# Kernel optimization log

Hardware: AMD Instinct MI355X
Metric: run time of the kernel (lower is better)

Reference implementation:

```python
import jax, jax.numpy as jnp
import numpy as np

B, N, D = 4, 4096, 1024
QK = D // 8          # qk_dim_div = 8 -> 128
E = 2 * D            # expand_factor = 2 -> 2048


def setup_inputs() -> dict:
    key = jax.random.key(0)
    k1, k2, k3 = jax.random.split(key, 3)
    x = jax.random.normal(k1, (B, N, D), dtype=jnp.float32)
    # xavier-uniform-like scale for the fused expand / project weights
    expand = jax.random.normal(k2, (D, 2 * QK + 2 * E), dtype=jnp.float32) * np.sqrt(2.0 / (D + 2 * QK + 2 * E)).astype(np.float32)
    project = jax.random.normal(k3, (E, D), dtype=jnp.float32) * np.sqrt(2.0 / (E + D)).astype(np.float32)
    position_bias_mult = jnp.float32(4.0)
    return {"x": x, "expand": expand, "project": project, "position_bias_mult": position_bias_mult}


def _layer_norm(x, eps=1e-5):
    mu = jnp.mean(x, axis=-1, keepdims=True)
    var = jnp.mean(jnp.square(x - mu), axis=-1, keepdims=True)
    return (x - mu) * jax.lax.rsqrt(var + eps)


def reference(x, expand, project, position_bias_mult):
    d = x.shape[-1]
    qk, e = d // 8, 2 * d
    n = x.shape[1]

    nx = _layer_norm(x)
    h = nx @ expand                                    # [B, N, 2*qk + 2*e]
    q = h[..., :qk]
    k = h[..., qk:2 * qk]
    linear = h[..., 2 * qk:2 * qk + e]
    pre_gelu = h[..., 2 * qk + e:]

    gated = linear * jax.nn.gelu(pre_gelu, approximate=False)  # torch F.gelu = exact erf
    local = gated[..., :e - d]                          # [B, N, e-d]
    v = gated[..., e - d:]                              # [B, N, d]

    # learned sigmoid position bias under causal mask
    pos = jnp.arange(n)
    base = (pos[None, :] - pos[:, None]).astype(x.dtype)  # j - i
    causal = pos[None, :] <= pos[:, None]
    mask = jnp.where(causal, jax.nn.sigmoid(base + position_bias_mult), -jnp.inf)

    logits = jnp.einsum('bnq,bmq->bnm', q, k) / np.sqrt(qk).astype(np.float32) + mask
    scores = jax.nn.softmax(logits, axis=-1)            # [B, N, N]
    attn = jnp.einsum('bnm,bmd->bnd', scores, v)         # [B, N, d]

    return x + jnp.concatenate([local, attn], axis=-1) @ project
```

## Files before the change

kernel.cpp:

```cpp
#include <hip/hip_runtime.h>
#include <type_traits>

typedef __bf16 bf16x8 __attribute__((ext_vector_type(8)));
typedef __bf16 bf16x4v __attribute__((ext_vector_type(4)));
typedef float f32x4 __attribute__((ext_vector_type(4)));
typedef unsigned short u16x8 __attribute__((ext_vector_type(8)));
typedef unsigned short u16x4 __attribute__((ext_vector_type(4)));

#define NSEQ 4096
#define DM 1024
#define NBATCH 4

__device__ __forceinline__ unsigned short f2bf(float f) {
  unsigned u = __float_as_uint(f);
  u += 0x7FFFu + ((u >> 16) & 1u);
  return (unsigned short)(u >> 16);
}
__device__ __forceinline__ float bf2f(unsigned short h) {
  return __uint_as_float(((unsigned)h) << 16);
}
__device__ __forceinline__ float gelu_exact(float x) {
  return 0.5f * x * (1.0f + erff(x * 0.7071067811865475f));
}

__device__ __forceinline__ void gload_lds16(const unsigned short* src,
                                            unsigned short* dst) {
  __builtin_amdgcn_global_load_lds(
      (const __attribute__((address_space(1))) unsigned int*)src,
      (__attribute__((address_space(3))) unsigned int*)dst, 16, 0, 0);
}

#define BAR() asm volatile("s_barrier" ::: "memory")
#define VMCNT8() asm volatile("s_waitcnt vmcnt(8)" ::: "memory")

__global__ __launch_bounds__(256) void ln_kernel(const float* __restrict__ x,
                                                 unsigned short* __restrict__ nx) {
  const int row = blockIdx.x;
  const int tid = threadIdx.x;
  const float4 v = reinterpret_cast<const float4*>(x + (size_t)row * DM)[tid];
  float s = v.x + v.y + v.z + v.w;
  float q = v.x * v.x + v.y * v.y + v.z * v.z + v.w * v.w;
#pragma unroll
  for (int off = 32; off > 0; off >>= 1) {
    s += __shfl_down(s, off);
    q += __shfl_down(q, off);
  }
  __shared__ float ss[4], sq[4];
  if ((tid & 63) == 0) {
    ss[tid >> 6] = s;
    sq[tid >> 6] = q;
  }
  __syncthreads();
  const float ts = ss[0] + ss[1] + ss[2] + ss[3];
  const float tq = sq[0] + sq[1] + sq[2] + sq[3];
  const float mu = ts * (1.0f / DM);
  const float var = tq * (1.0f / DM) - mu * mu;
  const float rs = rsqrtf(var + 1e-5f);
  u16x4 o;
  o[0] = f2bf((v.x - mu) * rs);
  o[1] = f2bf((v.y - mu) * rs);
  o[2] = f2bf((v.z - mu) * rs);
  o[3] = f2bf((v.w - mu) * rs);
  *reinterpret_cast<u16x4*>(nx + (size_t)row * DM + tid * 4) = o;
}

__global__ __launch_bounds__(256) void tconv_kernel(const float* __restrict__ in,
                                                    unsigned short* __restrict__ out,
                                                    int K, int N) {
  __shared__ unsigned short tile[64][72];
  const int n0 = blockIdx.x * 64;
  const int k0 = blockIdx.y * 64;
  const int tid = threadIdx.x;
  const int lr = tid >> 4, lc = (tid & 15) * 4;
#pragma unroll
  for (int p = 0; p < 4; p++) {
    const int r = lr + p * 16;
    float4 v = *reinterpret_cast<const float4*>(in + (size_t)(k0 + r) * N + n0 + lc);
    tile[r][lc + 0] = f2bf(v.x);
    tile[r][lc + 1] = f2bf(v.y);
    tile[r][lc + 2] = f2bf(v.z);
    tile[r][lc + 3] = f2bf(v.w);
  }
  __syncthreads();
  const int nn = tid >> 2, kkg = (tid & 3) * 16;
  u16x8 o0, o1;
#pragma unroll
  for (int j = 0; j < 8; j++) {
    o0[j] = tile[kkg + j][nn];
    o1[j] = tile[kkg + 8 + j][nn];
  }
  unsigned short* dst = out + (size_t)(n0 + nn) * K + k0 + kkg;
  *reinterpret_cast<u16x8*>(dst) = o0;
  *reinterpret_cast<u16x8*>(dst + 8) = o1;
}

template <bool FINAL>
__global__ __launch_bounds__(512, 2) void gemm256_kernel(
    const unsigned short* __restrict__ A, int lda,
    const unsigned short* __restrict__ Bt, int ldb, void* __restrict__ Cv,
    int ldc, int K, int ntn, const float* __restrict__ X) {
  __shared__ unsigned short Ah[2][2][8192];
  __shared__ unsigned short Bh[2][2][8192];
  const int tid = threadIdx.x;
  const int lane = tid & 63;
  const int w = tid >> 6;
  const int lq = lane & 15;
  const int lg = lane >> 4;
  const int wm = w >> 2;
  const int wn = w & 3;
  const int bid = blockIdx.x;
  const int m0 = (bid / ntn) * 256;
  const int n0 = (bid % ntn) * 256;
  const int nk = K >> 6;

  const int g0 = w * 64 + lane;
  const int rowS = g0 >> 2;
  const int kcS = ((g0 & 3) * 8) ^ (((rowS >> 1) & 3) << 3);
  const unsigned short* Asrc = A + (size_t)(m0 + rowS) * lda + kcS;
  const unsigned short* Bsrc = Bt + (size_t)(n0 + rowS) * ldb + kcS;
  const size_t ldaj = (size_t)128 * lda;
  const size_t ldbj = (size_t)128 * ldb;
  const int dstW = w * 64 * 8;

  auto stageA = [&](int db, int kh, int kt2) {
    if (kt2 < nk) {
      const unsigned short* s = Asrc + (size_t)kt2 * 64 + kh * 32;
      unsigned short* d = &Ah[db][kh][0] + dstW;
      gload_lds16(s, d);
      gload_lds16(s + ldaj, d + 4096);
    }
  };
  auto stageB = [&](int db, int kh, int kt2) {
    if (kt2 < nk) {
      const unsigned short* s = Bsrc + (size_t)kt2 * 64 + kh * 32;
      unsigned short* d = &Bh[db][kh][0] + dstW;
      gload_lds16(s, d);
      gload_lds16(s + ldbj, d + 4096);
    }
  };

  f32x4 acc[8][4];
#pragma unroll
  for (int i = 0; i < 8; i++)
#pragma unroll
    for (int j = 0; j < 4; j++)
#pragma unroll
      for (int r = 0; r < 4; r++) acc[i][j][r] = 0.0f;

  stageA(0, 0, 0);
  stageB(0, 0, 0);
  stageA(0, 1, 0);
  stageB(0, 1, 0);
  stageA(1, 0, 1);
  stageB(1, 0, 1);
  VMCNT8();
  BAR();

  const int aBase = wm * 128;
  const int bBase = wn * 64;
  const int cSwz = (lg * 8) ^ (((lq >> 1) & 3) << 3);

#pragma unroll 1
  for (int kt = 0; kt < nk; ++kt) {
    const int buf = kt & 1;
    bf16x8 af[4], bf0[4], bf1[4];

#pragma unroll
    for (int i = 0; i < 4; i++)
      af[i] = *reinterpret_cast<const bf16x8*>(
          &Ah[buf][0][(aBase + i * 16 + lq) * 32 + cSwz]);
#pragma unroll
    for (int j = 0; j < 4; j++)
      bf0[j] = *reinterpret_cast<const bf16x8*>(
          &Bh[buf][0][(bBase + j * 16 + lq) * 32 + cSwz]);
    stageA(buf ^ 1, 1, kt + 1);
    BAR();
    __builtin_amdgcn_s_setprio(1);
#pragma unroll
    for (int i = 0; i < 4; i++)
#pragma unroll
      for (int j = 0; j < 4; j++)
        acc[i][j] =
            __builtin_amdgcn_mfma_f32_16x16x32_bf16(af[i], bf0[j], acc[i][j], 0, 0, 0);
    __builtin_amdgcn_s_setprio(0);
    BAR();

#pragma unroll
    for (int i = 0; i < 4; i++)
      af[i] = *reinterpret_cast<const bf16x8*>(
          &Ah[buf][0][(aBase + 64 + i * 16 + lq) * 32 + cSwz]);
    stageB(buf ^ 1, 1, kt + 1);
    VMCNT8();
    BAR();
    __builtin_amdgcn_s_setprio(1);
#pragma unroll
    for (int i = 0; i < 4; i++)
#pragma unroll
      for (int j = 0; j < 4; j++)
        acc[4 + i][j] = __builtin_amdgcn_mfma_f32_16x16x32_bf16(af[i], bf0[j],
                                                                acc[4 + i][j], 0, 0, 0);
    __builtin_amdgcn_s_setprio(0);
    BAR();

#pragma unroll
    for (int i = 0; i < 4; i++)
      af[i] = *reinterpret_cast<const bf16x8*>(
          &Ah[buf][1][(aBase + i * 16 + lq) * 32 + cSwz]);
#pragma unroll
    for (int j = 0; j < 4; j++)
      bf1[j] = *reinterpret_cast<const bf16x8*>(
          &Bh[buf][1][(bBase + j * 16 + lq) * 32 + cSwz]);
    stageA(buf, 0, kt + 2);
    BAR();
    __builtin_amdgcn_s_setprio(1);
#pragma unroll
    for (int i = 0; i < 4; i++)
#pragma unroll
      for (int j = 0; j < 4; j++)
        acc[i][j] =
            __builtin_amdgcn_mfma_f32_16x16x32_bf16(af[i], bf1[j], acc[i][j], 0, 0, 0);
    __builtin_amdgcn_s_setprio(0);
    BAR();

#pragma unroll
    for (int i = 0; i < 4; i++)
      af[i] = *reinterpret_cast<const bf16x8*>(
          &Ah[buf][1][(aBase + 64 + i * 16 + lq) * 32 + cSwz]);
    stageB(buf, 0, kt + 2);
    VMCNT8();
    BAR();
    __builtin_amdgcn_s_setprio(1);
#pragma unroll
    for (int i = 0; i < 4; i++)
#pragma unroll
      for (int j = 0; j < 4; j++)
        acc[4 + i][j] = __builtin_amdgcn_mfma_f32_16x16x32_bf16(af[i], bf1[j],
                                                                acc[4 + i][j], 0, 0, 0);
    __builtin_amdgcn_s_setprio(0);
    BAR();
  }

  if (FINAL) {
    float* C = reinterpret_cast<float*>(Cv);
#pragma unroll
    for (int I = 0; I < 8; I++)
#pragma unroll
      for (int j = 0; j < 4; j++)
#pragma unroll
        for (int r = 0; r < 4; r++) {
          const int row = m0 + wm * 128 + I * 16 + lg * 4 + r;
          const int col = n0 + wn * 64 + j * 16 + lq;
          const size_t off = (size_t)row * ldc + col;
          C[off] = X[off] + acc[I][j][r];
        }
  } else {
    unsigned short* C = reinterpret_cast<unsigned short*>(Cv);
#pragma unroll
    for (int I = 0; I < 8; I++)
#pragma unroll
      for (int j = 0; j < 4; j++)
#pragma unroll
        for (int r = 0; r < 4; r++) {
          const int row = m0 + wm * 128 + I * 16 + lg * 4 + r;
          const int col = n0 + wn * 64 + j * 16 + lq;
          C[(size_t)row * ldc + col] = f2bf(acc[I][j][r]);
        }
  }
}

__global__ __launch_bounds__(256) void gate_local_kernel(
    const unsigned short* __restrict__ gateH, unsigned short* __restrict__ concat) {
  const int idx = blockIdx.x * 256 + threadIdx.x;
  const int row = idx >> 7;
  const int cg = idx & 127;
  const unsigned short* hr = gateH + (size_t)row * 4096;
  u16x8 lin = *reinterpret_cast<const u16x8*>(hr + cg * 8);
  u16x8 pg = *reinterpret_cast<const u16x8*>(hr + 2048 + cg * 8);
  u16x8 o;
#pragma unroll
  for (int j = 0; j < 8; j++) {
    const float l = bf2f(lin[j]);
    const float g = gelu_exact(bf2f(pg[j]));
    o[j] = f2bf(l * g);
  }
  *reinterpret_cast<u16x8*>(concat + (size_t)row * 2048 + cg * 8) = o;
}

__global__ __launch_bounds__(256) void gate_vt_kernel(
    const unsigned short* __restrict__ gateH, unsigned short* __restrict__ vT) {
  __shared__ unsigned short tbuf[64][72];
  const int n0 = blockIdx.x * 64;
  const int d0 = blockIdx.y * 64;
  const int b = blockIdx.z;
  const int tid = threadIdx.x;
#pragma unroll
  for (int p = 0; p < 2; p++) {
    const int r = p * 32 + (tid >> 3);
    const int cg = tid & 7;
    const unsigned short* hr = gateH + (size_t)(b * NSEQ + n0 + r) * 4096;
    u16x8 lin = *reinterpret_cast<const u16x8*>(hr + 1024 + d0 + cg * 8);
    u16x8 pg = *reinterpret_cast<const u16x8*>(hr + 3072 + d0 + cg * 8);
    u16x8 o;
#pragma unroll
    for (int j = 0; j < 8; j++) {
      const float l = bf2f(lin[j]);
      const float g = gelu_exact(bf2f(pg[j]));
      o[j] = f2bf(l * g);
    }
    *reinterpret_cast<u16x8*>(&tbuf[r][cg * 8]) = o;
  }
  __syncthreads();
#pragma unroll
  for (int p = 0; p < 2; p++) {
    const int d = p * 32 + (tid >> 3);
    const int ng = tid & 7;
    u16x8 o;
#pragma unroll
    for (int j = 0; j < 8; j++) o[j] = tbuf[ng * 8 + j][d];
    *reinterpret_cast<u16x8*>(vT + (size_t)(b * DM + d0 + d) * NSEQ + n0 +
                              ng * 8) = o;
  }
}

#define P_TILE 16384
#define P_PER_B 8650752
__global__ __launch_bounds__(512, 4) void pk_kernel(
    const unsigned short* __restrict__ qk, const float* __restrict__ pbm_ptr,
    unsigned short* __restrict__ P, float* __restrict__ l) {
  __shared__ unsigned short Ks[128][136];
  const int tid = threadIdx.x;
  const int lane = tid & 63;
  const int w = tid >> 6;
  const int lq = lane & 15;
  const int lg = lane >> 4;
  const int bid = blockIdx.x;
  const int b = bid / 528;
  const int t = bid - b * 528;
  int qt = (int)((sqrtf((float)(8 * t + 1)) - 1.0f) * 0.5f);
  while ((qt + 1) * (qt + 2) / 2 <= t) ++qt;
  while (qt * (qt + 1) / 2 > t) --qt;
  const int kt = t - qt * (qt + 1) / 2;
  const float pbm = *pbm_ptr;
  const float SCALE = 0.08838834764831845f;

  const unsigned short* qb = qk + (size_t)b * NSEQ * 256;

#pragma unroll
  for (int p = 0; p < 4; p++) {
    const int task = tid + p * 512;
    const int row = task >> 4;
    const int ch = task & 15;
    bf16x8 v = *reinterpret_cast<const bf16x8*>(
        qb + (size_t)(kt * 128 + row) * 256 + 128 + ch * 8);
    *reinterpret_cast<bf16x8*>(&Ks[row][ch * 8]) = v;
  }
  const int qloc = w * 16 + lq;
  bf16x8 qf[4];
#pragma unroll
  for (int ks = 0; ks < 4; ks++)
    qf[ks] = *reinterpret_cast<const bf16x8*>(
        qb + (size_t)(qt * 128 + qloc) * 256 + ks * 32 + lg * 8);
  __syncthreads();

  f32x4 sa[8];
#pragma unroll
  for (int sub = 0; sub < 8; sub++)
#pragma unroll
    for (int r = 0; r < 4; r++) sa[sub][r] = 0.0f;
#pragma unroll
  for (int ks = 0; ks < 4; ks++)
#pragma unroll
    for (int sub = 0; sub < 8; sub++) {
      bf16x8 kf =
          *reinterpret_cast<const bf16x8*>(&Ks[sub * 16 + lq][ks * 32 + lg * 8]);
      sa[sub] = __builtin_amdgcn_mfma_f32_16x16x32_bf16(kf, qf[ks], sa[sub], 0, 0, 0);
    }
  const size_t KL = (size_t)(qt + 1) * 128;
  unsigned short* Prow = P + (size_t)b * P_PER_B +
                         (size_t)(qt * (qt + 1) / 2) * P_TILE + (size_t)qloc * KL +
                         kt * 128;
  float ps = 0.0f;
  const bool diag = (kt == qt);
#pragma unroll
  for (int sub = 0; sub < 8; sub++) {
    bf16x4v pv;
#pragma unroll
    for (int r = 0; r < 4; r++) {
      const int kvloc = sub * 16 + lg * 4 + r;
      float p;
      if (diag && kvloc > qloc) {
        p = 0.0f;
      } else {
        const float dn = (float)((kt - qt) * 128 + kvloc - qloc) + pbm;
        const float s = sa[sub][r] * SCALE + 1.0f / (1.0f + __expf(-dn));
        p = __expf(s);
      }
      ps += p;
      pv[r] = (__bf16)p;
    }
    *reinterpret_cast<bf16x4v*>(Prow + sub * 16 + lg * 4) = pv;
  }
  ps += __shfl_xor(ps, 16);
  ps += __shfl_xor(ps, 32);
  if (lane < 16) atomicAdd(&l[b * NSEQ + qt * 128 + w * 16 + lane], ps);
}

__global__ __launch_bounds__(256, 4) void pv_kernel(
    const unsigned short* __restrict__ P, const unsigned short* __restrict__ vT,
    const float* __restrict__ l, unsigned short* __restrict__ concat) {
  __shared__ unsigned short As[128][64];
  __shared__ unsigned short Bs[128][64];
  const int tid = threadIdx.x;
  const int bid = blockIdx.x;
  const int qt = 31 - (bid >> 5);
  const int rest = bid & 31;
  const int b = rest >> 3;
  const int nt = rest & 7;
  const int KL = (qt + 1) * 128;
  const unsigned short* A =
      P + (size_t)b * P_PER_B + (size_t)(qt * (qt + 1) / 2) * P_TILE;
  const unsigned short* Bt = vT + (size_t)b * DM * NSEQ;
  const int n0 = nt * 128;
  const int lane = tid & 63;
  const int w = tid >> 6;
  const int lr = lane & 15;
  const int lg = lane >> 4;
  const int wr = (w >> 1) * 64;
  const int wc = (w & 1) * 64;
  const int rSwz = (lr & 7) << 3;

  f32x4 acc[4][4];
#pragma unroll
  for (int i = 0; i < 4; i++)
#pragma unroll
    for (int j = 0; j < 4; j++)
#pragma unroll
      for (int r = 0; r < 4; r++) acc[i][j][r] = 0.0f;

  for (int k0 = 0; k0 < KL; k0 += 64) {
#pragma unroll
    for (int j = 0; j < 4; j++) {
      const int boff = w * 4096 + j * 1024 + lane * 16;
      const int row = boff >> 7;
      const int col = (((boff & 127) >> 1)) ^ ((row & 7) << 3);
      gload_lds16(A + (size_t)row * KL + k0 + col,
                  &As[0][0] + (boff - lane * 16) / 2);
    }
#pragma unroll
    for (int j = 0; j < 4; j++) {
      const int boff = w * 4096 + j * 1024 + lane * 16;
      const int row = boff >> 7;
      const int col = (((boff & 127) >> 1)) ^ ((row & 7) << 3);
      gload_lds16(Bt + (size_t)(n0 + row) * NSEQ + k0 + col,
                  &Bs[0][0] + (boff - lane * 16) / 2);
    }
    __syncthreads();
#pragma unroll
    for (int kk = 0; kk < 64; kk += 32) {
      bf16x8 af[4], bfr[4];
#pragma unroll
      for (int i = 0; i < 4; i++)
        af[i] = *reinterpret_cast<const bf16x8*>(
            &As[wr + i * 16 + lr][(kk + lg * 8) ^ rSwz]);
#pragma unroll
      for (int j = 0; j < 4; j++)
        bfr[j] = *reinterpret_cast<const bf16x8*>(
            &Bs[wc + j * 16 + lr][(kk + lg * 8) ^ rSwz]);
#pragma unroll
      for (int i = 0; i < 4; i++)
#pragma unroll
        for (int j = 0; j < 4; j++)
          acc[i][j] = __builtin_amdgcn_mfma_f32_16x16x32_bf16(af[i], bfr[j],
                                                              acc[i][j], 0, 0, 0);
    }
    __syncthreads();
  }

  const float* lb = l + b * NSEQ + qt * 128;
#pragma unroll
  for (int i = 0; i < 4; i++) {
    f32x4 lv = *reinterpret_cast<const f32x4*>(&lb[wr + i * 16 + lg * 4]);
    f32x4 inv;
#pragma unroll
    for (int r = 0; r < 4; r++) inv[r] = 1.0f / lv[r];
#pragma unroll
    for (int j = 0; j < 4; j++)
#pragma unroll
      for (int r = 0; r < 4; r++) {
        const int grow = b * NSEQ + qt * 128 + wr + i * 16 + lg * 4 + r;
        const int col = 1024 + n0 + wc + j * 16 + lr;
        concat[(size_t)grow * 2048 + col] = f2bf(acc[i][j][r] * inv[r]);
      }
  }
}

extern "C" void kernel_launch(void* const* d_in, const int* in_sizes, int n_in,
                              void* d_out, int out_size, void* d_ws,
                              size_t ws_size, hipStream_t stream) {
  (void)in_sizes;
  (void)n_in;
  (void)out_size;
  const float* x = (const float*)d_in[0];
  const float* expand = (const float*)d_in[1];
  const float* project = (const float*)d_in[2];
  const float* pbm = (const float*)d_in[3];
  float* out = (float*)d_out;

  const size_t QK_BYTES = (size_t)16384 * 256 * 2;
  const size_t GH_BYTES = (size_t)16384 * 4096 * 2;
  const size_t CAT_BYTES = (size_t)16384 * 2048 * 2;
  const size_t NX_BYTES = (size_t)16384 * DM * 2;
  const size_t P_BYTES = (size_t)NBATCH * P_PER_B * 2;
  if (ws_size < QK_BYTES + GH_BYTES + CAT_BYTES + NX_BYTES) return;

  char* ws = (char*)d_ws;
  unsigned short* qk = (unsigned short*)ws;
  unsigned short* gateH = (unsigned short*)(ws + QK_BYTES);
  unsigned short* concat = (unsigned short*)(ws + QK_BYTES + GH_BYTES);
  unsigned short* nx = (unsigned short*)(ws + QK_BYTES + GH_BYTES + CAT_BYTES);
  unsigned short* vT = nx;
  unsigned short* projectT = nx;
  unsigned short* expandT = concat;
  unsigned short* P = gateH;
  float* l = (float*)(ws + QK_BYTES + P_BYTES);

  tconv_kernel<<<dim3(68, 16), 256, 0, stream>>>(expand, expandT, 1024, 4352);
  ln_kernel<<<16384, 256, 0, stream>>>(x, nx);
  gemm256_kernel<false><<<dim3(64), 512, 0, stream>>>(
      nx, DM, expandT, DM, (void*)qk, 256, DM, 1, nullptr);
  gemm256_kernel<false><<<dim3(64 * 16), 512, 0, stream>>>(
      nx, DM, expandT + (size_t)256 * DM, DM, (void*)gateH, 4096, DM, 16, nullptr);
  gate_local_kernel<<<8192, 256, 0, stream>>>(gateH, concat);
  gate_vt_kernel<<<dim3(64, 16, 4), 256, 0, stream>>>(gateH, vT);
  hipMemsetAsync(l, 0, (size_t)NBATCH * NSEQ * 4, stream);
  pk_kernel<<<dim3(NBATCH * 528), 512, 0, stream>>>(qk, pbm, P, l);
  pv_kernel<<<dim3(1024), 256, 0, stream>>>(P, vT, l, concat);
  tconv_kernel<<<dim3(16, 32), 256, 0, stream>>>(project, projectT, 2048, DM);
  gemm256_kernel<true><<<dim3(64 * 4), 512, 0, stream>>>(
      concat, 2048, projectT, 2048, (void*)out, DM, 2048, 4, x);
}
```

Measured before the change: 478.0 us.

## Prefetch LDS fragments one phase ahead and remap blocks across XCDs

Restructures the GEMM main loop so LDS-to-register fragment loads for the next MFMA phase are issued right after the barrier and overlap the current phase's MFMAs, using two alternating register sets (Ax/Ay, Ba/Bb). The aim is to hide LDS read latency behind matrix-core work. It also remaps blockIdx so consecutive tiles land on the same XCD (8-way interleave) for better L2 reuse. Extra live fragment registers raise pressure, which could cause spills under the 512-thread, 2-blocks-per-CU launch bounds. The remap assumes the grid size is a multiple of 8.

```diff
diff --git a/kernel.cpp b/kernel.cpp
--- a/kernel.cpp
+++ b/kernel.cpp
@@ -108,7 +108,8 @@
   const int lg = lane >> 4;
   const int wm = w >> 2;
   const int wn = w & 3;
-  const int bid = blockIdx.x;
+  const int cpx = gridDim.x >> 3;
+  const int bid = (blockIdx.x & 7) * cpx + (blockIdx.x >> 3);
   const int m0 = (bid / ntn) * 256;
   const int n0 = (bid % ntn) * 256;
   const int nk = K >> 6;
@@ -139,6 +140,23 @@
     }
   };
 
+  const int aBase = wm * 128;
+  const int bBase = wn * 64;
+  const int cSwz = (lg * 8) ^ (((lq >> 1) & 3) << 3);
+
+  auto loadA = [&](bf16x8* dst, int bufI, int kh, int rbase) {
+#pragma unroll
+    for (int i = 0; i < 4; i++)
+      dst[i] = *reinterpret_cast<const bf16x8*>(
+          &Ah[bufI][kh][(rbase + i * 16 + lq) * 32 + cSwz]);
+  };
+  auto loadB = [&](bf16x8* dst, int bufI, int kh) {
+#pragma unroll
+    for (int j = 0; j < 4; j++)
+      dst[j] = *reinterpret_cast<const bf16x8*>(
+          &Bh[bufI][kh][(bBase + j * 16 + lq) * 32 + cSwz]);
+  };
+
   f32x4 acc[8][4];
 #pragma unroll
   for (int i = 0; i < 8; i++)
@@ -146,6 +164,8 @@
     for (int j = 0; j < 4; j++)
 #pragma unroll
       for (int r = 0; r < 4; r++) acc[i][j][r] = 0.0f;
+
+  bf16x8 Ax[4], Ay[4], Ba[4], Bb[4];
 
   stageA(0, 0, 0);
   stageB(0, 0, 0);
@@ -155,86 +175,65 @@
   stageB(1, 0, 1);
   VMCNT8();
   BAR();
-
-  const int aBase = wm * 128;
-  const int bBase = wn * 64;
-  const int cSwz = (lg * 8) ^ (((lq >> 1) & 3) << 3);
+  loadA(Ax, 0, 0, aBase);
+  loadB(Ba, 0, 0);
 
 #pragma unroll 1
   for (int kt = 0; kt < nk; ++kt) {
     const int buf = kt & 1;
-    bf16x8 af[4], bf0[4], bf1[4];
-
+
+    stageA(buf ^ 1, 1, kt + 1);
+    BAR();
+    loadA(Ay, buf, 0, aBase + 64);
+    __builtin_amdgcn_s_setprio(1);
 #pragma unroll
     for (int i = 0; i < 4; i++)
-      af[i] = *reinterpret_cast<const bf16x8*>(
-          &Ah[buf][0][(aBase + i * 16 + lq) * 32 + cSwz]);
-#pragma unroll
-    for (int j = 0; j < 4; j++)
-      bf0[j] = *reinterpret_cast<const bf16x8*>(
-          &Bh[buf][0][(bBase + j * 16 + lq) * 32 + cSwz]);
-    stageA(buf ^ 1, 1, kt + 1);
-    BAR();
-    __builtin_amdgcn_s_setprio(1);
-#pragma unroll
-    for (int i = 0; i < 4; i++)
 #pragma unroll
       for (int j = 0; j < 4; j++)
         acc[i][j] =
-            __builtin_amdgcn_mfma_f32_16x16x32_bf16(af[i], bf0[j], acc[i][j], 0, 0, 0);
+            __builtin_amdgcn_mfma_f32_16x16x32_bf16(Ax[i], Ba[j], acc[i][j], 0, 0, 0);
     __builtin_amdgcn_s_setprio(0);
     BAR();
 
-#pragma unroll
-    for (int i = 0; i < 4; i++)
-      af[i] = *reinterpret_cast<const bf16x8*>(
-          &Ah[buf][0][(aBase + 64 + i * 16 + lq) * 32 + cSwz]);
     stageB(buf ^ 1, 1, kt + 1);
     VMCNT8();
     BAR();
+    loadA(Ax, buf, 1, aBase);
+    loadB(Bb, buf, 1);
     __builtin_amdgcn_s_setprio(1);
 #pragma unroll
     for (int i = 0; i < 4; i++)
 #pragma unroll
       for (int j = 0; j < 4; j++)
-        acc[4 + i][j] = __builtin_amdgcn_mfma_f32_16x16x32_bf16(af[i], bf0[j],
+        acc[4 + i][j] = __builtin_amdgcn_mfma_f32_16x16x32_bf16(Ay[i], Ba[j],
                                                                 acc[4 + i][j], 0, 0, 0);
     __builtin_amdgcn_s_setprio(0);
     BAR();
 
+    stageA(buf, 0, kt + 2);
+    BAR();
+    loadA(Ay, buf, 1, aBase + 64);
+    __builtin_amdgcn_s_setprio(1);
 #pragma unroll
     for (int i = 0; i < 4; i++)
-      af[i] = *reinterpret_cast<const bf16x8*>(
-          &Ah[buf][1][(aBase + i * 16 + lq) * 32 + cSwz]);
-#pragma unroll
-    for (int j = 0; j < 4; j++)
-      bf1[j] = *reinterpret_cast<const bf16x8*>(
-          &Bh[buf][1][(bBase + j * 16 + lq) * 32 + cSwz]);
-    stageA(buf, 0, kt + 2);
-    BAR();
-    __builtin_amdgcn_s_setprio(1);
-#pragma unroll
-    for (int i = 0; i < 4; i++)
 #pragma unroll
       for (int j = 0; j < 4; j++)
         acc[i][j] =
-            __builtin_amdgcn_mfma_f32_16x16x32_bf16(af[i], bf1[j], acc[i][j], 0, 0, 0);
+            __builtin_amdgcn_mfma_f32_16x16x32_bf16(Ax[i], Bb[j], acc[i][j], 0, 0, 0);
     __builtin_amdgcn_s_setprio(0);
     BAR();
 
-#pragma unroll
-    for (int i = 0; i < 4; i++)
-      af[i] = *reinterpret_cast<const bf16x8*>(
-          &Ah[buf][1][(aBase + 64 + i * 16 + lq) * 32 + cSwz]);
     stageB(buf, 0, kt + 2);
     VMCNT8();
     BAR();
+    loadA(Ax, buf ^ 1, 0, aBase);
+    loadB(Ba, buf ^ 1, 0);
     __builtin_amdgcn_s_setprio(1);
 #pragma unroll
     for (int i = 0; i < 4; i++)
 #pragma unroll
       for (int j = 0; j < 4; j++)
-        acc[4 + i][j] = __builtin_amdgcn_mfma_f32_16x16x32_bf16(af[i], bf1[j],
+        acc[4 + i][j] = __builtin_amdgcn_mfma_f32_16x16x32_bf16(Ay[i], Bb[j],
                                                                 acc[4 + i][j], 0, 0, 0);
     __builtin_amdgcn_s_setprio(0);
     BAR();
```

New measurement: 490.6 us. +2.6%, slower.

## Fuse GELU gating into expand GEMM epilogue via interleaved weight columns

Applied to the files above, without the earlier changes.

The transposed expand weights get their linear and pre-gelu columns interleaved in 32-column groups. Each 64-wide warp tile of the gate GEMM then holds matching linear and gate values, so the epilogue computes linear*gelu directly and writes local features to concat and v to a compact buffer. This drops the 16384x4096 bf16 intermediate round trip and the separate gating kernels, leaving a pure transpose kernel for v. The cost is a heavier GEMM epilogue with erf, scattered 2-byte stores, and a reshuffled workspace layout.

```diff
diff --git a/kernel.cpp b/kernel.cpp
--- a/kernel.cpp
+++ b/kernel.cpp
@@ -32,6 +32,14 @@
 
 #define BAR() asm volatile("s_barrier" ::: "memory")
 #define VMCNT8() asm volatile("s_waitcnt vmcnt(8)" ::: "memory")
+
+__device__ __forceinline__ int perm_col(int n) {
+  if (n < 256) return n;
+  int c = n - 256;
+  if (c < 2048) return 256 + ((c >> 5) << 6) + (c & 31);
+  c -= 2048;
+  return 256 + ((c >> 5) << 6) + 32 + (c & 31);
+}
 
 __global__ __launch_bounds__(256) void ln_kernel(const float* __restrict__ x,
                                                  unsigned short* __restrict__ nx) {
@@ -64,6 +72,7 @@
   *reinterpret_cast<u16x4*>(nx + (size_t)row * DM + tid * 4) = o;
 }
 
+template <bool PERM>
 __global__ __launch_bounds__(256) void tconv_kernel(const float* __restrict__ in,
                                                     unsigned short* __restrict__ out,
                                                     int K, int N) {
@@ -89,16 +98,18 @@
     o0[j] = tile[kkg + j][nn];
     o1[j] = tile[kkg + 8 + j][nn];
   }
-  unsigned short* dst = out + (size_t)(n0 + nn) * K + k0 + kkg;
+  const int orow = PERM ? perm_col(n0 + nn) : (n0 + nn);
+  unsigned short* dst = out + (size_t)orow * K + k0 + kkg;
   *reinterpret_cast<u16x8*>(dst) = o0;
   *reinterpret_cast<u16x8*>(dst + 8) = o1;
 }
 
-template <bool FINAL>
+template <int MODE>
 __global__ __launch_bounds__(512, 2) void gemm256_kernel(
     const unsigned short* __restrict__ A, int lda,
     const unsigned short* __restrict__ Bt, int ldb, void* __restrict__ Cv,
-    int ldc, int K, int ntn, const float* __restrict__ X) {
+    void* __restrict__ Cv2, int ldc, int K, int ntn,
+    const float* __restrict__ X) {
   __shared__ unsigned short Ah[2][2][8192];
   __shared__ unsigned short Bh[2][2][8192];
   const int tid = threadIdx.x;
@@ -240,7 +251,7 @@
     BAR();
   }
 
-  if (FINAL) {
+  if (MODE == 1) {
     float* C = reinterpret_cast<float*>(Cv);
 #pragma unroll
     for (int I = 0; I < 8; I++)
@@ -253,7 +264,7 @@
           const size_t off = (size_t)row * ldc + col;
           C[off] = X[off] + acc[I][j][r];
         }
-  } else {
+  } else if (MODE == 0) {
     unsigned short* C = reinterpret_cast<unsigned short*>(Cv);
 #pragma unroll
     for (int I = 0; I < 8; I++)
@@ -265,29 +276,31 @@
           const int col = n0 + wn * 64 + j * 16 + lq;
           C[(size_t)row * ldc + col] = f2bf(acc[I][j][r]);
         }
-  }
-}
-
-__global__ __launch_bounds__(256) void gate_local_kernel(
-    const unsigned short* __restrict__ gateH, unsigned short* __restrict__ concat) {
-  const int idx = blockIdx.x * 256 + threadIdx.x;
-  const int row = idx >> 7;
-  const int cg = idx & 127;
-  const unsigned short* hr = gateH + (size_t)row * 4096;
-  u16x8 lin = *reinterpret_cast<const u16x8*>(hr + cg * 8);
-  u16x8 pg = *reinterpret_cast<const u16x8*>(hr + 2048 + cg * 8);
-  u16x8 o;
-#pragma unroll
-  for (int j = 0; j < 8; j++) {
-    const float l = bf2f(lin[j]);
-    const float g = gelu_exact(bf2f(pg[j]));
-    o[j] = f2bf(l * g);
-  }
-  *reinterpret_cast<u16x8*>(concat + (size_t)row * 2048 + cg * 8) = o;
-}
-
-__global__ __launch_bounds__(256) void gate_vt_kernel(
-    const unsigned short* __restrict__ gateH, unsigned short* __restrict__ vT) {
+  } else {
+    unsigned short* concat = reinterpret_cast<unsigned short*>(Cv);
+    unsigned short* vbuf = reinterpret_cast<unsigned short*>(Cv2);
+    const int pi = (n0 + wn * 64) >> 6;
+    const int cBase = pi * 32;
+#pragma unroll
+    for (int I = 0; I < 8; I++)
+#pragma unroll
+      for (int j = 0; j < 2; j++) {
+        const int c = cBase + j * 16 + lq;
+#pragma unroll
+        for (int r = 0; r < 4; r++) {
+          const int row = m0 + wm * 128 + I * 16 + lg * 4 + r;
+          const float g = acc[I][j][r] * gelu_exact(acc[I][j + 2][r]);
+          if (c < 1024)
+            concat[(size_t)row * 2048 + c] = f2bf(g);
+          else
+            vbuf[(size_t)row * 1024 + (c - 1024)] = f2bf(g);
+        }
+      }
+  }
+}
+
+__global__ __launch_bounds__(256) void vt_kernel(
+    const unsigned short* __restrict__ vbuf, unsigned short* __restrict__ vT) {
   __shared__ unsigned short tbuf[64][72];
   const int n0 = blockIdx.x * 64;
   const int d0 = blockIdx.y * 64;
@@ -297,17 +310,9 @@
   for (int p = 0; p < 2; p++) {
     const int r = p * 32 + (tid >> 3);
     const int cg = tid & 7;
-    const unsigned short* hr = gateH + (size_t)(b * NSEQ + n0 + r) * 4096;
-    u16x8 lin = *reinterpret_cast<const u16x8*>(hr + 1024 + d0 + cg * 8);
-    u16x8 pg = *reinterpret_cast<const u16x8*>(hr + 3072 + d0 + cg * 8);
-    u16x8 o;
-#pragma unroll
-    for (int j = 0; j < 8; j++) {
-      const float l = bf2f(lin[j]);
-      const float g = gelu_exact(bf2f(pg[j]));
-      o[j] = f2bf(l * g);
-    }
-    *reinterpret_cast<u16x8*>(&tbuf[r][cg * 8]) = o;
+    u16x8 v = *reinterpret_cast<const u16x8*>(
+        vbuf + (size_t)(b * NSEQ + n0 + r) * 1024 + d0 + cg * 8);
+    *reinterpret_cast<u16x8*>(&tbuf[r][cg * 8]) = v;
   }
   __syncthreads();
 #pragma unroll
@@ -507,35 +512,38 @@
   float* out = (float*)d_out;
 
   const size_t QK_BYTES = (size_t)16384 * 256 * 2;
+  const size_t VBUF_BYTES = (size_t)16384 * 1024 * 2;
+  const size_t P_BYTES = (size_t)NBATCH * P_PER_B * 2;
+  const size_t L_BYTES = (size_t)NBATCH * NSEQ * 4;
   const size_t GH_BYTES = (size_t)16384 * 4096 * 2;
   const size_t CAT_BYTES = (size_t)16384 * 2048 * 2;
   const size_t NX_BYTES = (size_t)16384 * DM * 2;
-  const size_t P_BYTES = (size_t)NBATCH * P_PER_B * 2;
   if (ws_size < QK_BYTES + GH_BYTES + CAT_BYTES + NX_BYTES) return;
 
   char* ws = (char*)d_ws;
   unsigned short* qk = (unsigned short*)ws;
-  unsigned short* gateH = (unsigned short*)(ws + QK_BYTES);
+  unsigned short* vbuf = (unsigned short*)(ws + QK_BYTES);
+  unsigned short* P = (unsigned short*)(ws + QK_BYTES + VBUF_BYTES);
+  float* l = (float*)(ws + QK_BYTES + VBUF_BYTES + P_BYTES);
+  unsigned short* expandT =
+      (unsigned short*)(ws + QK_BYTES + VBUF_BYTES + P_BYTES + L_BYTES);
   unsigned short* concat = (unsigned short*)(ws + QK_BYTES + GH_BYTES);
   unsigned short* nx = (unsigned short*)(ws + QK_BYTES + GH_BYTES + CAT_BYTES);
   unsigned short* vT = nx;
   unsigned short* projectT = nx;
-  unsigned short* expandT = concat;
-  unsigned short* P = gateH;
-  float* l = (float*)(ws + QK_BYTES + P_BYTES);
-
-  tconv_kernel<<<dim3(68, 16), 256, 0, stream>>>(expand, expandT, 1024, 4352);
+
+  tconv_kernel<true><<<dim3(68, 16), 256, 0, stream>>>(expand, expandT, 1024, 4352);
   ln_kernel<<<16384, 256, 0, stream>>>(x, nx);
-  gemm256_kernel<false><<<dim3(64), 512, 0, stream>>>(
-      nx, DM, expandT, DM, (void*)qk, 256, DM, 1, nullptr);
-  gemm256_kernel<false><<<dim3(64 * 16), 512, 0, stream>>>(
-      nx, DM, expandT + (size_t)256 * DM, DM, (void*)gateH, 4096, DM, 16, nullptr);
-  gate_local_kernel<<<8192, 256, 0, stream>>>(gateH, concat);
-  gate_vt_kernel<<<dim3(64, 16, 4), 256, 0, stream>>>(gateH, vT);
-  hipMemsetAsync(l, 0, (size_t)NBATCH * NSEQ * 4, stream);
+  gemm256_kernel<0><<<dim3(64), 512, 0, stream>>>(
+      nx, DM, expandT, DM, (void*)qk, nullptr, 256, DM, 1, nullptr);
+  gemm256_kernel<2><<<dim3(64 * 16), 512, 0, stream>>>(
+      nx, DM, expandT + (size_t)256 * DM, DM, (void*)concat, (void*)vbuf, 0, DM,
+      16, nullptr);
+  vt_kernel<<<dim3(64, 16, 4), 256, 0, stream>>>(vbuf, vT);
+  hipMemsetAsync(l, 0, L_BYTES, stream);
   pk_kernel<<<dim3(NBATCH * 528), 512, 0, stream>>>(qk, pbm, P, l);
   pv_kernel<<<dim3(1024), 256, 0, stream>>>(P, vT, l, concat);
-  tconv_kernel<<<dim3(16, 32), 256, 0, stream>>>(project, projectT, 2048, DM);
-  gemm256_kernel<true><<<dim3(64 * 4), 512, 0, stream>>>(
-      concat, 2048, projectT, 2048, (void*)out, DM, 2048, 4, x);
-}
+  tconv_kernel<false><<<dim3(16, 32), 256, 0, stream>>>(project, projectT, 2048, DM);
+  gemm256_kernel<1><<<dim3(64 * 4), 512, 0, stream>>>(
+      concat, 2048, projectT, 2048, (void*)out, nullptr, DM, 2048, 4, x);
+}
```

Measured after the change: 471.6 us. Within noise of the previous version (-1.3%).
